# Performance work log

Measured on AMD Instinct MI355X. Metric: run time of the kernel, lower is better.

## Reference

```python
import jax, jax.numpy as jnp
import numpy as np

NG, ND = 50000, 20000
EG, ED = 300000, 150000
FG = FD = 256
H = 256
FC = 2048
B = 65536
EPS = 1e-5


def _lrelu(x):
    return jnp.where(x >= 0, x, 0.01 * x)


def _bn(x, g, b):
    # BatchNorm1d in training mode: biased batch stats over the node dim
    m = x.mean(axis=0)
    v = ((x - m) ** 2).mean(axis=0)
    return (x - m) * jax.lax.rsqrt(v + EPS) * g + b


def _gconv(x, edge_index, Wr, br, Ws, n_nodes):
    # PyG GraphConv: out = lin_rel(sum_{j->i} x_j) + lin_root(x_i)
    src, dst = edge_index[0], edge_index[1]
    agg = jax.ops.segment_sum(x[src], dst, num_segments=n_nodes)  # [N, in]
    return agg @ Wr + br + x @ Ws


def setup_inputs() -> dict:
    key = jax.random.key(0)
    ks = iter(jax.random.split(key, 64))
    d = {}
    d["gene_x"] = jax.random.normal(next(ks), (NG, FG), jnp.float32)
    d["disease_x"] = jax.random.normal(next(ks), (ND, FD), jnp.float32)
    d["gene_edge_index"] = jax.random.randint(next(ks), (2, EG), 0, NG, jnp.int32)
    d["disease_edge_index"] = jax.random.randint(next(ks), (2, ED), 0, ND, jnp.int32)
    d["batch_idx"] = jax.random.randint(next(ks), (B, 2), 0, ND, jnp.int32)

    def lin(fin, fout):
        s = 1.0 / np.sqrt(fin)
        W = jax.random.uniform(next(ks), (fin, fout), jnp.float32, -s, s)
        b = jax.random.uniform(next(ks), (fout,), jnp.float32, -s, s)
        return W, b

    for p, fin in (("g", FG), ("d", FD)):
        for i in range(3):
            f = fin if i == 0 else H
            Wr, br = lin(f, H)
            Ws, _ = lin(f, H)
            d[f"{p}{i}_Wr"], d[f"{p}{i}_br"], d[f"{p}{i}_Ws"] = Wr, br, Ws
            d[f"bn{p}{i}_g"] = jnp.ones((H,), jnp.float32)
            d[f"bn{p}{i}_b"] = jnp.zeros((H,), jnp.float32)
    d["lin1_W"], d["lin1_b"] = lin(2 * H, FC)
    d["lin2_W"], d["lin2_b"] = lin(FC, FC // 2)
    d["lin3_W"], d["lin3_b"] = lin(FC // 2, FC // 4)
    d["lin4_W"], d["lin4_b"] = lin(FC // 4, 2)
    return d


def reference(gene_x, disease_x, gene_edge_index, disease_edge_index, batch_idx,
              g0_Wr, g0_br, g0_Ws, g1_Wr, g1_br, g1_Ws, g2_Wr, g2_br, g2_Ws,
              d0_Wr, d0_br, d0_Ws, d1_Wr, d1_br, d1_Ws, d2_Wr, d2_br, d2_Ws,
              bng0_g, bng0_b, bng1_g, bng1_b, bng2_g, bng2_b,
              bnd0_g, bnd0_b, bnd1_g, bnd1_b, bnd2_g, bnd2_b,
              lin1_W, lin1_b, lin2_W, lin2_b, lin3_W, lin3_b, lin4_W, lin4_b):
    # gene tower
    g0 = _bn(_lrelu(_gconv(gene_x, gene_edge_index, g0_Wr, g0_br, g0_Ws, NG)), bng0_g, bng0_b)
    g1 = _bn(_lrelu(_gconv(g0, gene_edge_index, g1_Wr, g1_br, g1_Ws, NG)), bng1_g, bng1_b)
    g2 = _bn(_lrelu(_gconv(g1, gene_edge_index, g2_Wr, g2_br, g2_Ws, NG)), bng2_g, bng2_b)
    gene_out = 0.7 * g0 + 0.2 * g1 + 0.1 * g2
    # disease tower
    h0 = _bn(_lrelu(_gconv(disease_x, disease_edge_index, d0_Wr, d0_br, d0_Ws, ND)), bnd0_g, bnd0_b)
    h1 = _bn(_lrelu(_gconv(h0, disease_edge_index, d1_Wr, d1_br, d1_Ws, ND)), bnd1_g, bnd1_b)
    h2 = _bn(_lrelu(_gconv(h1, disease_edge_index, d2_Wr, d2_br, d2_Ws, ND)), bnd2_g, bnd2_b)
    dis_out = 0.7 * h0 + 0.2 * h1 + 0.1 * h2
    # pair gather + MLP head (dropout is identity in eval)
    x = jnp.concatenate([gene_out[batch_idx[:, 0]], dis_out[batch_idx[:, 1]]], axis=1)
    x = _lrelu(x @ lin1_W + lin1_b)
    x = _lrelu(x @ lin2_W + lin2_b)
    x = _lrelu(x @ lin3_W + lin3_b)
    return x @ lin4_W + lin4_b
```

## Files before the change

### kernel.cpp

```cpp
#include <hip/hip_runtime.h>
#include <hip/hip_bf16.h>
#include <cstdint>
#include <cstddef>

#define N_G 50000
#define N_D 20000
#define E_G 300000
#define E_D 150000
#define BATCH 65536

typedef _Float16 f16;
typedef _Float16 f16x8 __attribute__((ext_vector_type(8)));
typedef _Float16 f16x4 __attribute__((ext_vector_type(4)));
typedef float f32x4 __attribute__((ext_vector_type(4)));

__device__ __forceinline__ float clampf(float v) {
    return fminf(fmaxf(v, -60000.f), 60000.f);
}

__device__ __forceinline__ void gl_lds16(const void* g, void* l) {
    __builtin_amdgcn_global_load_lds(
        (const __attribute__((address_space(1))) unsigned int*)g,
        (__attribute__((address_space(3))) unsigned int*)l, 16, 0, 0);
}

__global__ __launch_bounds__(256) void gemm_f16(
    const f16* __restrict__ A,
    const int* __restrict__ bidx,
    const f16* __restrict__ geneT, const f16* __restrict__ disT, int rowBase,
    const f16* __restrict__ Bt, const float* __restrict__ bias,
    f16* __restrict__ C, int M, int N, int K, int relu, int CB, int RB,
    const float* __restrict__ W4, float* __restrict__ outF)
{
    alignas(16) __shared__ f16 sA[128 * 64];
    alignas(16) __shared__ f16 sB[128 * 64];
    const int t = threadIdx.x;
    const int w = t >> 6, l = t & 63;
    const int wm = w >> 1, wn = w & 1;
    const int q = l >> 4, lr = l & 15;

    int flat = blockIdx.x;
    int cb, rb;
    if ((RB & 7) == 0) {
        int x = flat & 7, idx = flat >> 3;
        int Sx = RB >> 3;
        cb = idx % CB;
        rb = x * Sx + idx / CB;
    } else {
        cb = flat % CB;
        rb = flat / CB;
    }
    const int mBase = rb * 128, nBase = cb * 128;

    const int subrow = l >> 3;
    const int c = l & 7;
    const char* pA[4];
    const char* pD[4];
    const char* pB[4];
    const bool fused = (bidx != nullptr);
    const bool concat = (!fused && disT != nullptr);
    const bool twoSrc = fused || concat;
#pragma unroll
    for (int j = 0; j < 4; j++) {
        int seg = j * 4 + w;
        int lrow = seg * 8 + subrow;
        int coff = ((c ^ (lrow & 7)) << 4);
        if (fused) {
            int rg = rowBase + mBase + lrow;
            int gi = bidx[2 * rg], di = bidx[2 * rg + 1];
            pA[j] = (const char*)geneT + (size_t)gi * 512 + coff;
            pD[j] = (const char*)disT + (size_t)di * 512 + coff;
        } else if (concat) {
            int arow = mBase + lrow; if (arow > M - 1) arow = M - 1;
            pA[j] = (const char*)geneT + (size_t)arow * 512 + coff;
            pD[j] = (const char*)disT + (size_t)arow * 512 + coff;
        } else {
            int arow = mBase + lrow; if (arow > M - 1) arow = M - 1;
            pA[j] = (const char*)A + (size_t)arow * K * 2 + coff;
            pD[j] = nullptr;
        }
        int brow = nBase + lrow; if (brow > N - 1) brow = N - 1;
        pB[j] = (const char*)Bt + (size_t)brow * K * 2 + coff;
    }

    f32x4 acc[4][4] = {};

    for (int k0 = 0; k0 < K; k0 += 64) {
        __syncthreads();
#pragma unroll
        for (int j = 0; j < 4; j++) {
            int seg = j * 4 + w;
            const char* srcA;
            if (twoSrc)
                srcA = (k0 < 256) ? (pA[j] + (size_t)k0 * 2) : (pD[j] + (size_t)(k0 - 256) * 2);
            else
                srcA = pA[j] + (size_t)k0 * 2;
            gl_lds16(srcA, sA + seg * 512);
            gl_lds16(pB[j] + (size_t)k0 * 2, sB + seg * 512);
        }
        __syncthreads();
        f16x8 a0[4], a1[4], b0[4], b1[4];
#pragma unroll
        for (int i = 0; i < 4; i++) {
            int r = wm * 64 + i * 16 + lr;
            int rs = r * 64;
            int x0 = (q ^ (r & 7)) << 3;
            int x1 = ((4 + q) ^ (r & 7)) << 3;
            a0[i] = *(const f16x8*)(sA + rs + x0);
            a1[i] = *(const f16x8*)(sA + rs + x1);
        }
#pragma unroll
        for (int jj = 0; jj < 4; jj++) {
            int r = wn * 64 + jj * 16 + lr;
            int rs = r * 64;
            int x0 = (q ^ (r & 7)) << 3;
            int x1 = ((4 + q) ^ (r & 7)) << 3;
            b0[jj] = *(const f16x8*)(sB + rs + x0);
            b1[jj] = *(const f16x8*)(sB + rs + x1);
        }
#pragma unroll
        for (int i = 0; i < 4; i++)
#pragma unroll
            for (int jj = 0; jj < 4; jj++) {
                acc[i][jj] = __builtin_amdgcn_mfma_f32_16x16x32_f16(a0[i], b0[jj], acc[i][jj], 0, 0, 0);
                acc[i][jj] = __builtin_amdgcn_mfma_f32_16x16x32_f16(a1[i], b1[jj], acc[i][jj], 0, 0, 0);
            }
    }

    if (W4 != nullptr) {
        float w40[4], w41[4];
#pragma unroll
        for (int j = 0; j < 4; j++) {
            int col = nBase + wn * 64 + j * 16 + lr;
            w40[j] = W4[col * 2];
            w41[j] = W4[col * 2 + 1];
        }
#pragma unroll
        for (int i = 0; i < 4; i++) {
#pragma unroll
            for (int r = 0; r < 4; r++) {
                int row = mBase + wm * 64 + i * 16 + q * 4 + r;
                float s0 = 0.f, s1 = 0.f;
#pragma unroll
                for (int j = 0; j < 4; j++) {
                    int col = nBase + wn * 64 + j * 16 + lr;
                    float v = acc[i][j][r] + bias[col];
                    v = v >= 0.f ? v : 0.01f * v;
                    v = clampf(v);
                    s0 += v * w40[j];
                    s1 += v * w41[j];
                }
#pragma unroll
                for (int off = 1; off < 16; off <<= 1) {
                    s0 += __shfl_xor(s0, off);
                    s1 += __shfl_xor(s1, off);
                }
                if (lr == 0 && row < M) {
                    atomicAdd(&outF[(size_t)(rowBase + row) * 2], s0);
                    atomicAdd(&outF[(size_t)(rowBase + row) * 2 + 1], s1);
                }
            }
        }
        return;
    }

    __syncthreads();
    f16* lt = ((w >> 1) ? sB : sA) + (w & 1) * 4096;

    float bj[4];
#pragma unroll
    for (int j = 0; j < 4; j++)
        bj[j] = bias ? bias[nBase + wn * 64 + j * 16 + lr] : 0.f;

#pragma unroll
    for (int i = 0; i < 4; i++)
#pragma unroll
        for (int j = 0; j < 4; j++) {
            int col = j * 16 + lr;
#pragma unroll
            for (int r = 0; r < 4; r++) {
                int row = i * 16 + q * 4 + r;
                float v = acc[i][j][r] + bj[j];
                if (relu) v = v >= 0.f ? v : 0.01f * v;
                v = clampf(v);
                int cs = col ^ ((((row >> 2) & 3) << 4) ^ ((row & 3) << 3));
                lt[row * 64 + cs] = (f16)v;
            }
        }
    __syncthreads();

    const int rr = l >> 3;
    const int c8 = l & 7;
#pragma unroll
    for (int it = 0; it < 8; it++) {
        int row = it * 8 + rr;
        int cs = (c8 * 8) ^ ((((row >> 2) & 3) << 4) ^ ((row & 3) << 3));
        f16x8 vv = *(const f16x8*)(lt + row * 64 + cs);
        int grow = mBase + wm * 64 + row;
        if (grow < M)
            *(f16x8*)(C + (size_t)grow * N + nBase + wn * 64 + c8 * 8) = vv;
    }
}

__global__ __launch_bounds__(512) void gemm256(
    const f16* __restrict__ A,
    const int* __restrict__ bidx,
    const f16* __restrict__ geneT, const f16* __restrict__ disT, int rowBase,
    const f16* __restrict__ Bt, const float* __restrict__ bias,
    f16* __restrict__ C, int M, int N, int K, int relu, int CB, int RB)
{
    alignas(16) __shared__ f16 sm[81920];
    const int t = threadIdx.x;
    const int w = t >> 6, l = t & 63;
    const int wm = w >> 2, wn = w & 3;
    const int q = l >> 4, lr = l & 15;

    int flat = blockIdx.x;
    int cb, rb;
    if ((RB & 7) == 0) {
        int x = flat & 7, idx = flat >> 3;
        int Sx = RB >> 3;
        cb = idx % CB;
        rb = x * Sx + idx / CB;
    } else {
        cb = flat % CB;
        rb = flat / CB;
    }
    const int mBase = rb * 256, nBase = cb * 256;

    const int subrow = l >> 3;
    const int c = l & 7;
    const bool gat = (bidx != nullptr);
    const char* pA[4];
    const char* pD[4];
    const char* pB[4];
#pragma unroll
    for (int jj = 0; jj < 4; jj++) {
        int arow = jj * 64 + w * 8 + subrow;
        int coff = ((c ^ (arow & 7)) << 4);
        if (gat) {
            int rg = rowBase + mBase + arow;
            int gi = bidx[2 * rg], di = bidx[2 * rg + 1];
            pA[jj] = (const char*)geneT + (size_t)gi * 512 + coff;
            pD[jj] = (const char*)disT + (size_t)di * 512 + coff;
        } else {
            int ga = mBase + arow; if (ga > M - 1) ga = M - 1;
            pA[jj] = (const char*)A + (size_t)ga * K * 2 + coff;
            pD[jj] = nullptr;
        }
        int gb = nBase + arow; if (gb > N - 1) gb = N - 1;
        pB[jj] = (const char*)Bt + (size_t)gb * K * 2 + coff;
    }

    f16* const smA = sm;
    f16* const smB = sm + 3 * 16384;

    auto stageA = [&](int abuf, int k0) {
        f16* bA = smA + abuf * 16384;
#pragma unroll
        for (int jj = 0; jj < 4; jj++) {
            int R0 = jj * 64 + w * 8;
            const char* srcA;
            if (gat)
                srcA = (k0 < 256) ? (pA[jj] + (size_t)k0 * 2) : (pD[jj] + (size_t)(k0 - 256) * 2);
            else
                srcA = pA[jj] + (size_t)k0 * 2;
            gl_lds16(srcA, bA + R0 * 64);
        }
    };
    auto stageB = [&](int bbuf, int k0) {
        f16* bB = smB + bbuf * 16384;
#pragma unroll
        for (int jj = 0; jj < 4; jj++) {
            int R0 = jj * 64 + w * 8;
            gl_lds16(pB[jj] + (size_t)k0 * 2, bB + R0 * 64);
        }
    };

    f32x4 acc[8][4] = {};
    const int nkt = K >> 6;

    stageA(0, 0);
    stageB(0, 0);
    if (nkt > 1) stageA(1, 64);

    for (int kt = 0; kt < nkt; kt++) {
        if (kt + 1 < nkt) stageB((kt + 1) & 1, (kt + 1) << 6);
        if (kt + 2 < nkt) stageA((kt + 2) % 3, (kt + 2) << 6);
        if (kt + 2 < nkt)      asm volatile("s_waitcnt vmcnt(12)" ::: "memory");
        else if (kt + 1 < nkt) asm volatile("s_waitcnt vmcnt(8)" ::: "memory");
        else                   asm volatile("s_waitcnt vmcnt(0)" ::: "memory");
        __builtin_amdgcn_s_barrier();
        __builtin_amdgcn_sched_barrier(0);
        const f16* bA = smA + (kt % 3) * 16384;
        const f16* bB = smB + (kt & 1) * 16384;
#pragma unroll
        for (int ks = 0; ks < 2; ks++) {
            f16x8 bf[4];
#pragma unroll
            for (int nf = 0; nf < 4; nf++) {
                int rB = wn * 64 + nf * 16 + lr;
                bf[nf] = *(const f16x8*)(bB + rB * 64 + ((((ks << 2) + q) ^ (rB & 7)) << 3));
            }
#pragma unroll
            for (int mf = 0; mf < 8; mf++) {
                int rA = wm * 128 + mf * 16 + lr;
                f16x8 af = *(const f16x8*)(bA + rA * 64 + ((((ks << 2) + q) ^ (rA & 7)) << 3));
#pragma unroll
                for (int nf = 0; nf < 4; nf++)
                    acc[mf][nf] = __builtin_amdgcn_mfma_f32_16x16x32_f16(af, bf[nf], acc[mf][nf], 0, 0, 0);
            }
        }
        __builtin_amdgcn_sched_barrier(0);
        __builtin_amdgcn_s_barrier();
    }
    __builtin_amdgcn_sched_barrier(0);

    f16* lt = sm + w * 8192;
    float bj[4];
#pragma unroll
    for (int nf = 0; nf < 4; nf++)
        bj[nf] = bias ? bias[nBase + wn * 64 + nf * 16 + lr] : 0.f;

#pragma unroll
    for (int mf = 0; mf < 8; mf++)
#pragma unroll
        for (int nf = 0; nf < 4; nf++) {
            int col = nf * 16 + lr;
#pragma unroll
            for (int r = 0; r < 4; r++) {
                int row = mf * 16 + q * 4 + r;
                float v = acc[mf][nf][r] + bj[nf];
                if (relu) v = v >= 0.f ? v : 0.01f * v;
                v = clampf(v);
                int cs = col ^ ((((row >> 2) & 3) << 4) ^ ((row & 3) << 3));
                lt[row * 64 + cs] = (f16)v;
            }
        }

    const int rr = l >> 3;
    const int c8 = l & 7;
#pragma unroll
    for (int it = 0; it < 16; it++) {
        int row = it * 8 + rr;
        int cs = (c8 * 8) ^ ((((row >> 2) & 3) << 4) ^ ((row & 3) << 3));
        f16x8 vv = *(const f16x8*)(lt + row * 64 + cs);
        int grow = mBase + wm * 128 + row;
        if (grow < M)
            *(f16x8*)(C + (size_t)grow * N + nBase + wn * 64 + c8 * 8) = vv;
    }
}

__global__ __launch_bounds__(256) void gemm_tower2(
    const f16* __restrict__ Xg, const f16* __restrict__ XAg,
    const f16* __restrict__ Btg, const float* __restrict__ biasg,
    f16* __restrict__ Cg, int Mg, int RBg, float* __restrict__ statsg,
    const f16* __restrict__ Xd, const f16* __restrict__ XAd,
    const f16* __restrict__ Btd, const float* __restrict__ biasd,
    f16* __restrict__ Cd, int Md, int RBd, float* __restrict__ statsd)
{
    alignas(16) __shared__ f16 sA[128 * 64];
    alignas(16) __shared__ f16 sB[128 * 64];
    const int t = threadIdx.x;
    const int w = t >> 6, l = t & 63;
    const int wm = w >> 1, wn = w & 1;
    const int q = l >> 4, lr = l & 15;

    int flat = blockIdx.x;
    const int geneBlocks = 2 * RBg;
    const f16* X;  const f16* XA;  const f16* Bt;  const float* bias;
    f16* C;  int M, RB;  float* stats;
    if (flat < geneBlocks) {
        X = Xg; XA = XAg; Bt = Btg; bias = biasg; C = Cg; M = Mg; RB = RBg; stats = statsg;
    } else {
        flat -= geneBlocks;
        X = Xd; XA = XAd; Bt = Btd; bias = biasd; C = Cd; M = Md; RB = RBd; stats = statsd;
    }

    int cb, rb;
    if ((RB & 7) == 0) {
        int x = flat & 7, idx = flat >> 3;
        int Sx = RB >> 3;
        cb = idx % 2;
        rb = x * Sx + idx / 2;
    } else {
        cb = flat % 2;
        rb = flat / 2;
    }
    const int mBase = rb * 128, nBase = cb * 128;

    const int subrow = l >> 3;
    const int c = l & 7;
    const char* pA[4];
    const char* pD[4];
    const char* pB[4];
#pragma unroll
    for (int j = 0; j < 4; j++) {
        int seg = j * 4 + w;
        int lrow = seg * 8 + subrow;
        int coff = ((c ^ (lrow & 7)) << 4);
        int arow = mBase + lrow; if (arow > M - 1) arow = M - 1;
        pA[j] = (const char*)X + (size_t)arow * 512 + coff;
        pD[j] = (const char*)XA + (size_t)arow * 512 + coff;
        int brow = nBase + lrow; if (brow > 255) brow = 255;
        pB[j] = (const char*)Bt + (size_t)brow * 1024 + coff;
    }

    f32x4 acc[4][4] = {};

    for (int k0 = 0; k0 < 512; k0 += 64) {
        __syncthreads();
#pragma unroll
        for (int j = 0; j < 4; j++) {
            int seg = j * 4 + w;
            const char* srcA = (k0 < 256) ? (pA[j] + (size_t)k0 * 2)
                                          : (pD[j] + (size_t)(k0 - 256) * 2);
            gl_lds16(srcA, sA + seg * 512);
            gl_lds16(pB[j] + (size_t)k0 * 2, sB + seg * 512);
        }
        __syncthreads();
        f16x8 a0[4], a1[4], b0[4], b1[4];
#pragma unroll
        for (int i = 0; i < 4; i++) {
            int r = wm * 64 + i * 16 + lr;
            int rs = r * 64;
            int x0 = (q ^ (r & 7)) << 3;
            int x1 = ((4 + q) ^ (r & 7)) << 3;
            a0[i] = *(const f16x8*)(sA + rs + x0);
            a1[i] = *(const f16x8*)(sA + rs + x1);
        }
#pragma unroll
        for (int jj = 0; jj < 4; jj++) {
            int r = wn * 64 + jj * 16 + lr;
            int rs = r * 64;
            int x0 = (q ^ (r & 7)) << 3;
            int x1 = ((4 + q) ^ (r & 7)) << 3;
            b0[jj] = *(const f16x8*)(sB + rs + x0);
            b1[jj] = *(const f16x8*)(sB + rs + x1);
        }
#pragma unroll
        for (int i = 0; i < 4; i++)
#pragma unroll
            for (int jj = 0; jj < 4; jj++) {
                acc[i][jj] = __builtin_amdgcn_mfma_f32_16x16x32_f16(a0[i], b0[jj], acc[i][jj], 0, 0, 0);
                acc[i][jj] = __builtin_amdgcn_mfma_f32_16x16x32_f16(a1[i], b1[jj], acc[i][jj], 0, 0, 0);
            }
    }

    __syncthreads();
    f16* lt = ((w >> 1) ? sB : sA) + (w & 1) * 4096;

    float bj[4];
#pragma unroll
    for (int j = 0; j < 4; j++)
        bj[j] = bias[nBase + wn * 64 + j * 16 + lr];

    float sj[4] = {0.f, 0.f, 0.f, 0.f}, s2j[4] = {0.f, 0.f, 0.f, 0.f};
#pragma unroll
    for (int i = 0; i < 4; i++)
#pragma unroll
        for (int j = 0; j < 4; j++) {
            int col = j * 16 + lr;
#pragma unroll
            for (int r = 0; r < 4; r++) {
                int row = i * 16 + q * 4 + r;
                float v = acc[i][j][r] + bj[j];
                v = v >= 0.f ? v : 0.01f * v;
                v = clampf(v);
                if ((mBase + wm * 64 + row) < M) { sj[j] += v; s2j[j] += v * v; }
                int cs = col ^ ((((row >> 2) & 3) << 4) ^ ((row & 3) << 3));
                lt[row * 64 + cs] = (f16)v;
            }
        }

#pragma unroll
    for (int j = 0; j < 4; j++) {
        float s = sj[j], s2 = s2j[j];
        s += __shfl_xor(s, 16); s2 += __shfl_xor(s2, 16);
        s += __shfl_xor(s, 32); s2 += __shfl_xor(s2, 32);
        if (q == 0) {
            int col = nBase + wn * 64 + j * 16 + lr;
            atomicAdd(&stats[col], s);
            atomicAdd(&stats[256 + col], s2);
        }
    }
    __syncthreads();

    const int rr = l >> 3;
    const int c8 = l & 7;
#pragma unroll
    for (int it = 0; it < 8; it++) {
        int row = it * 8 + rr;
        int cs = (c8 * 8) ^ ((((row >> 2) & 3) << 4) ^ ((row & 3) << 3));
        f16x8 vv = *(const f16x8*)(lt + row * 64 + cs);
        int grow = mBase + wm * 64 + row;
        if (grow < M)
            *(f16x8*)(C + (size_t)grow * 256 + nBase + wn * 64 + c8 * 8) = vv;
    }
}

__global__ void cvt2(const float* __restrict__ gx, const float* __restrict__ dx,
                     f16* __restrict__ og, f16* __restrict__ od) {
    size_t i = ((size_t)blockIdx.x * 256 + threadIdx.x) * 8;
    const size_t ng = (size_t)N_G * 256;
    const float* in; f16* out;
    if (i < ng) { in = gx + i; out = og + i; }
    else {
        size_t j = i - ng;
        if (j >= (size_t)N_D * 256) return;
        in = dx + j; out = od + j;
    }
    f32x4 a = *(const f32x4*)in;
    f32x4 b = *(const f32x4*)(in + 4);
    f16x8 o;
    o[0] = (f16)clampf(a.x); o[1] = (f16)clampf(a.y);
    o[2] = (f16)clampf(a.z); o[3] = (f16)clampf(a.w);
    o[4] = (f16)clampf(b.x); o[5] = (f16)clampf(b.y);
    o[6] = (f16)clampf(b.z); o[7] = (f16)clampf(b.w);
    *(f16x8*)out = o;
}

__global__ void init_out(const float* __restrict__ b4, float* __restrict__ out, int n) {
    int i = blockIdx.x * 256 + threadIdx.x;
    if (i < n) out[i] = b4[i & 1];
}

__global__ void count_deg2(const int* __restrict__ gei, const int* __restrict__ dei,
                           int* __restrict__ cntg, int* __restrict__ cntd) {
    int e = blockIdx.x * 256 + threadIdx.x;
    if (e < E_G) atomicAdd(&cntg[gei[E_G + e]], 1);
    else if (e < E_G + E_D) atomicAdd(&cntd[dei[E_D + (e - E_G)]], 1);
}

__global__ void scan_deg2(const int* __restrict__ cntg, int* __restrict__ rpg,
                          const int* __restrict__ cntd, int* __restrict__ rpd) {
    __shared__ int part[1024];
    const int t = threadIdx.x;
    const int* deg = blockIdx.x ? cntd : cntg;
    int* rowptr = blockIdx.x ? rpd : rpg;
    const int Nn = blockIdx.x ? N_D : N_G;
    const int C = (Nn + 1023) >> 10;
    const int base = t * C;
    int s = 0;
    for (int i = 0; i < C; i++) { int idx = base + i; if (idx < Nn) s += deg[idx]; }
    part[t] = s;
    __syncthreads();
    for (int off = 1; off < 1024; off <<= 1) {
        int v = (t >= off) ? part[t - off] : 0;
        __syncthreads();
        part[t] += v;
        __syncthreads();
    }
    int pre = (t == 0) ? 0 : part[t - 1];
    for (int i = 0; i < C; i++) {
        int idx = base + i;
        if (idx < Nn) { rowptr[idx] = pre; pre += deg[idx]; }
    }
    if (t == 1023) rowptr[Nn] = part[1023];
}

__global__ void fill_csr2(const int* __restrict__ gei, const int* __restrict__ dei,
                          const int* __restrict__ rpg, const int* __restrict__ rpd,
                          int* __restrict__ curg, int* __restrict__ curd,
                          int* __restrict__ csrg, int* __restrict__ csrd) {
    int e = blockIdx.x * 256 + threadIdx.x;
    if (e < E_G) {
        int d = gei[E_G + e];
        int p = rpg[d] + atomicAdd(&curg[d], 1);
        csrg[p] = gei[e];
    } else if (e < E_G + E_D) {
        int e2 = e - E_G;
        int d = dei[E_D + e2];
        int p = rpd[d] + atomicAdd(&curd[d], 1);
        csrd[p] = dei[e2];
    }
}

__global__ void agg_x2(const int* __restrict__ rpg, const int* __restrict__ csrg,
                       const f16* __restrict__ Xg, f16* __restrict__ XAg,
                       const int* __restrict__ rpd, const int* __restrict__ csrd,
                       const f16* __restrict__ Xd, f16* __restrict__ XAd) {
    int gid = blockIdx.x * 256 + threadIdx.x;
    int node = gid >> 6, l = gid & 63;
    const int* rowptr; const int* csr; const f16* X; f16* XA;
    if (node < N_G) { rowptr = rpg; csr = csrg; X = Xg; XA = XAg; }
    else {
        node -= N_G;
        if (node >= N_D) return;
        rowptr = rpd; csr = csrd; X = Xd; XA = XAd;
    }
    int beg = rowptr[node], end = rowptr[node + 1];
    float s0 = 0.f, s1 = 0.f, s2 = 0.f, s3 = 0.f;
    for (int e = beg; e < end; e++) {
        int src = csr[e];
        f16x4 xv = *(const f16x4*)(X + (size_t)src * 256 + l * 4);
        s0 += (float)xv.x; s1 += (float)xv.y; s2 += (float)xv.z; s3 += (float)xv.w;
    }
    f16x4 o;
    o.x = (f16)clampf(s0); o.y = (f16)clampf(s1);
    o.z = (f16)clampf(s2); o.w = (f16)clampf(s3);
    *(f16x4*)(XA + (size_t)node * 256 + l * 4) = o;
}

__global__ void bn_apply2(f16* __restrict__ yg, f16* __restrict__ yd,
                          const float* __restrict__ stg, const float* __restrict__ std_,
                          const float* __restrict__ gg, const float* __restrict__ bg,
                          const float* __restrict__ gd, const float* __restrict__ bd,
                          float invNg, float invNd, float wv,
                          f16* __restrict__ accg, f16* __restrict__ accd, int initAcc) {
    size_t i = ((size_t)blockIdx.x * 256 + threadIdx.x) * 8;
    const size_t ng = (size_t)N_G * 256;
    f16* y; f16* acc; const float* stats; const float* g; const float* b; float invN;
    if (i < ng) { y = yg + i; acc = accg + i; stats = stg; g = gg; b = bg; invN = invNg; }
    else {
        size_t j = i - ng;
        if (j >= (size_t)N_D * 256) return;
        y = yd + j; acc = accd + j; stats = std_; g = gd; b = bd; invN = invNd;
    }
    int colb = (int)(i & 255);
    f16x8 yv = *(const f16x8*)y;
    f16x8 av = {};
    if (!initAcc) av = *(const f16x8*)acc;
    f16x8 yo, ao;
#pragma unroll
    for (int j = 0; j < 8; j++) {
        int col = colb + j;
        float m = stats[col] * invN;
        float var = stats[256 + col] * invN - m * m;
        if (var < 0.f) var = 0.f;
        float rs = 1.0f / sqrtf(var + 1e-5f);
        float v = ((float)yv[j] - m) * rs * g[col] + b[col];
        v = clampf(v);
        yo[j] = (f16)v;
        float p = initAcc ? 0.f : (float)av[j];
        ao[j] = (f16)clampf(p + wv * v);
    }
    *(f16x8*)y = yo;
    *(f16x8*)acc = ao;
}

__global__ void transpose_tile(const float* __restrict__ W, f16* __restrict__ WT,
                               int K, int N, int dstRowOff, int dstColOff, int LK) {
    __shared__ float tile[32][33];
    int n0 = blockIdx.x * 32, k0 = blockIdx.y * 32;
    int tx = threadIdx.x, ty = threadIdx.y;
    for (int yy = ty; yy < 32; yy += 8) {
        int k = k0 + yy, n = n0 + tx;
        tile[yy][tx] = (k < K && n < N) ? W[(size_t)k * N + n] : 0.f;
    }
    __syncthreads();
    for (int yy = ty; yy < 32; yy += 8) {
        int n = n0 + yy, k = k0 + tx;
        if (n < N && k < K)
            WT[(size_t)(dstRowOff + n) * LK + dstColOff + k] = (f16)clampf(tile[tx][yy]);
    }
}

struct WPtrs { const float* p[12]; };
__global__ void transpose12(WPtrs wp, f16* __restrict__ WT) {
    __shared__ float tile[32][33];
    const int z = blockIdx.z;
    const float* W = wp.p[z];
    const int s = z >> 1;
    const int colOff = (z & 1) * 256;
    f16* dst = WT + (size_t)s * 131072;
    int n0 = blockIdx.x * 32, k0 = blockIdx.y * 32;
    int tx = threadIdx.x, ty = threadIdx.y;
    for (int yy = ty; yy < 32; yy += 8)
        tile[yy][tx] = W[(size_t)(k0 + yy) * 256 + n0 + tx];
    __syncthreads();
    for (int yy = ty; yy < 32; yy += 8)
        dst[(size_t)(n0 + yy) * 512 + colOff + k0 + tx] = (f16)clampf(tile[tx][yy]);
}

extern "C" void kernel_launch(void* const* d_in, const int* in_sizes, int n_in,
                              void* d_out, int out_size, void* d_ws, size_t ws_size,
                              hipStream_t stream) {
    char* ws = (char*)d_ws;
    size_t off = 0;
    auto alloc = [&](size_t bytes) -> void* {
        void* p = ws + off;
        off += (bytes + 255) & ~(size_t)255;
        return p;
    };

    f16* gene_out = (f16*)alloc((size_t)N_G * 256 * 2);
    f16* dis_out  = (f16*)alloc((size_t)N_D * 256 * 2);
    f16* W1T = (f16*)alloc((size_t)2048 * 512 * 2);
    f16* W2T = (f16*)alloc((size_t)1024 * 2048 * 2);
    f16* W3T = (f16*)alloc((size_t)512 * 1024 * 2);
    f16* WcatT = (f16*)alloc((size_t)6 * 256 * 512 * 2);
    int* csr_g = (int*)alloc((size_t)E_G * 4);
    int* csr_d = (int*)alloc((size_t)E_D * 4);
    int* rp_g = (int*)alloc((size_t)(N_G + 1) * 4);
    int* rp_d = (int*)alloc((size_t)(N_D + 1) * 4);
    int* cnt = (int*)alloc((size_t)(N_G + N_D) * 4);
    int* cnt_g = cnt;
    int* cnt_d = cnt + N_G;
    float* statsAll = (float*)alloc(6 * 512 * 4);

    char* scratch = ws + off;
    size_t avail = (ws_size > off) ? (ws_size - off) : 0;

    const size_t NSG = (size_t)N_G * 256;
    const size_t NSD = (size_t)N_D * 256;
    f16* gX = (f16*)scratch;
    f16* gY = gX + NSG;
    f16* gXA = gY + NSG;
    f16* dX = gXA + NSG;
    f16* dY = dX + NSD;
    f16* dXA = dY + NSD;

    int R = BATCH;
    while ((size_t)R * 6144 > avail && R > 256) R >>= 1;
    int chunks = BATCH / R;
    f16* h1 = (f16*)scratch;
    f16* h2 = h1 + (size_t)R * 2048;

    const float* gene_x = (const float*)d_in[0];
    const float* disease_x = (const float*)d_in[1];
    const int* g_ei = (const int*)d_in[2];
    const int* d_ei = (const int*)d_in[3];
    const int* bidx = (const int*)d_in[4];
    float* out = (float*)d_out;

    const float wl[3] = {0.7f, 0.2f, 0.1f};

    hipMemsetAsync(statsAll, 0, 6 * 512 * 4, stream);
    hipMemsetAsync(cnt, 0, (size_t)(N_G + N_D) * 4, stream);
    {
        size_t tot8 = ((NSG + NSD) / 8 + 255) / 256;
        cvt2<<<(int)tot8, 256, 0, stream>>>(gene_x, disease_x, gX, dX);
    }
    count_deg2<<<(E_G + E_D + 255) / 256, 256, 0, stream>>>(g_ei, d_ei, cnt_g, cnt_d);
    scan_deg2<<<2, 1024, 0, stream>>>(cnt_g, rp_g, cnt_d, rp_d);
    hipMemsetAsync(cnt, 0, (size_t)(N_G + N_D) * 4, stream);
    fill_csr2<<<(E_G + E_D + 255) / 256, 256, 0, stream>>>(g_ei, d_ei, rp_g, rp_d,
                                                           cnt_g, cnt_d, csr_g, csr_d);
    {
        WPtrs wp;
        for (int l = 0; l < 3; l++) {
            wp.p[l * 2 + 0] = (const float*)d_in[5 + l * 5 + 2];
            wp.p[l * 2 + 1] = (const float*)d_in[5 + l * 5 + 0];
            wp.p[6 + l * 2 + 0] = (const float*)d_in[20 + l * 5 + 2];
            wp.p[6 + l * 2 + 1] = (const float*)d_in[20 + l * 5 + 0];
        }
        transpose12<<<dim3(8, 8, 12), dim3(32, 8), 0, stream>>>(wp, WcatT);
    }

    const int RBg = ((N_G + 127) / 128 + 7) & ~7;
    const int RBd = ((N_D + 127) / 128 + 7) & ~7;
    f16* gIn = gX; f16* gOut = gY;
    f16* dIn = dX; f16* dOut = dY;
    int aggBlocks = ((N_G + N_D) * 64 + 255) / 256;
    int bnBlocks = (int)(((NSG + NSD) / 8 + 255) / 256);
    for (int l = 0; l < 3; l++) {
        const float* br_g = (const float*)d_in[5 + l * 5 + 1];
        const float* bg_g = (const float*)d_in[5 + l * 5 + 3];
        const float* bb_g = (const float*)d_in[5 + l * 5 + 4];
        const float* br_d = (const float*)d_in[20 + l * 5 + 1];
        const float* bg_d = (const float*)d_in[20 + l * 5 + 3];
        const float* bb_d = (const float*)d_in[20 + l * 5 + 4];
        agg_x2<<<aggBlocks, 256, 0, stream>>>(rp_g, csr_g, gIn, gXA,
                                              rp_d, csr_d, dIn, dXA);
        gemm_tower2<<<2 * RBg + 2 * RBd, 256, 0, stream>>>(
            gIn, gXA, WcatT + (size_t)l * 131072, br_g, gOut, N_G, RBg, statsAll + l * 512,
            dIn, dXA, WcatT + (size_t)(3 + l) * 131072, br_d, dOut, N_D, RBd,
            statsAll + (3 + l) * 512);
        bn_apply2<<<bnBlocks, 256, 0, stream>>>(gOut, dOut,
                                                statsAll + l * 512, statsAll + (3 + l) * 512,
                                                bg_g, bb_g, bg_d, bb_d,
                                                1.0f / N_G, 1.0f / N_D, wl[l],
                                                gene_out, dis_out, l == 0);
        f16* tmp = gIn; gIn = gOut; gOut = tmp;
        tmp = dIn; dIn = dOut; dOut = tmp;
    }

    const float* lin1_W = (const float*)d_in[35];
    const float* lin1_b = (const float*)d_in[36];
    const float* lin2_W = (const float*)d_in[37];
    const float* lin2_b = (const float*)d_in[38];
    const float* lin3_W = (const float*)d_in[39];
    const float* lin3_b = (const float*)d_in[40];
    const float* lin4_W = (const float*)d_in[41];
    const float* lin4_b = (const float*)d_in[42];

    transpose_tile<<<dim3(64, 16), dim3(32, 8), 0, stream>>>(lin1_W, W1T, 512, 2048, 0, 0, 512);
    transpose_tile<<<dim3(32, 64), dim3(32, 8), 0, stream>>>(lin2_W, W2T, 2048, 1024, 0, 0, 2048);
    transpose_tile<<<dim3(16, 32), dim3(32, 8), 0, stream>>>(lin3_W, W3T, 1024, 512, 0, 0, 1024);
    init_out<<<(BATCH * 2 + 255) / 256, 256, 0, stream>>>(lin4_b, out, BATCH * 2);

    for (int c = 0; c < chunks; c++) {
        int rb = c * R;
        int RB = R / 128;
        if ((R & 255) == 0) {
            int RB2 = R / 256;
            gemm256<<<8 * RB2, 512, 0, stream>>>(nullptr, bidx, gene_out, dis_out, rb,
                                                 W1T, lin1_b, h1, R, 2048, 512, 1, 8, RB2);
        } else {
            gemm_f16<<<16 * RB, 256, 0, stream>>>(nullptr, bidx, gene_out, dis_out, rb,
                                                  W1T, lin1_b, h1, R, 2048, 512, 1, 16, RB,
                                                  nullptr, nullptr);
        }
        gemm_f16<<<8 * RB, 256, 0, stream>>>(h1, nullptr, nullptr, nullptr, 0,
                                             W2T, lin2_b, h2, R, 1024, 2048, 1, 8, RB,
                                             nullptr, nullptr);
        gemm_f16<<<4 * RB, 256, 0, stream>>>(h2, nullptr, nullptr, nullptr, rb,
                                             W3T, lin3_b, nullptr, R, 512, 1024, 1, 4, RB,
                                             lin4_W, out);
    }
}
```

Baseline: 1.328 ms.

## Replace 256x256 pipelined lin1 GEMM with 128x512 wide-tile single-buffer kernel

The lin1 GEMM, which gathers gene and disease rows, now uses a 128x512 output tile per 512-thread block, with each wave covering all 128 rows and its own 64 columns. The old version used 256x256 tiles with triple/double-buffered async staging. Shared memory drops from 160KB to 80KB, which should allow more blocks per CU and reduce gathered A-row loads per output column. The cost is that the software pipelining across k-tiles is removed: loads and compute are now serialized by __syncthreads each iteration. The epilogue is also split into two halves so it fits in the smaller LDS.

```diff
diff --git a/kernel.cpp b/kernel.cpp
--- a/kernel.cpp
+++ b/kernel.cpp
@@ -202,18 +202,19 @@
     }
 }
 
-__global__ __launch_bounds__(512) void gemm256(
-    const f16* __restrict__ A,
+__global__ __launch_bounds__(512) void gemm_wide(
     const int* __restrict__ bidx,
     const f16* __restrict__ geneT, const f16* __restrict__ disT, int rowBase,
     const f16* __restrict__ Bt, const float* __restrict__ bias,
-    f16* __restrict__ C, int M, int N, int K, int relu, int CB, int RB)
+    f16* __restrict__ C, int M, int N, int K, int CB, int RB)
 {
-    alignas(16) __shared__ f16 sm[81920];
+    alignas(16) __shared__ f16 sm[40960];
+    f16* const sA = sm;
+    f16* const sB = sm + 8192;
     const int t = threadIdx.x;
     const int w = t >> 6, l = t & 63;
-    const int wm = w >> 2, wn = w & 3;
     const int q = l >> 4, lr = l & 15;
+    const int subrow = l >> 3, c = l & 7;
 
     int flat = blockIdx.x;
     int cb, rb;
@@ -226,128 +227,99 @@
         cb = flat % CB;
         rb = flat / CB;
     }
-    const int mBase = rb * 256, nBase = cb * 256;
-
-    const int subrow = l >> 3;
-    const int c = l & 7;
-    const bool gat = (bidx != nullptr);
-    const char* pA[4];
-    const char* pD[4];
-    const char* pB[4];
-#pragma unroll
-    for (int jj = 0; jj < 4; jj++) {
-        int arow = jj * 64 + w * 8 + subrow;
-        int coff = ((c ^ (arow & 7)) << 4);
-        if (gat) {
-            int rg = rowBase + mBase + arow;
-            int gi = bidx[2 * rg], di = bidx[2 * rg + 1];
-            pA[jj] = (const char*)geneT + (size_t)gi * 512 + coff;
-            pD[jj] = (const char*)disT + (size_t)di * 512 + coff;
-        } else {
-            int ga = mBase + arow; if (ga > M - 1) ga = M - 1;
-            pA[jj] = (const char*)A + (size_t)ga * K * 2 + coff;
-            pD[jj] = nullptr;
-        }
-        int gb = nBase + arow; if (gb > N - 1) gb = N - 1;
-        pB[jj] = (const char*)Bt + (size_t)gb * K * 2 + coff;
-    }
-
-    f16* const smA = sm;
-    f16* const smB = sm + 3 * 16384;
-
-    auto stageA = [&](int abuf, int k0) {
-        f16* bA = smA + abuf * 16384;
-#pragma unroll
-        for (int jj = 0; jj < 4; jj++) {
-            int R0 = jj * 64 + w * 8;
-            const char* srcA;
-            if (gat)
-                srcA = (k0 < 256) ? (pA[jj] + (size_t)k0 * 2) : (pD[jj] + (size_t)(k0 - 256) * 2);
-            else
-                srcA = pA[jj] + (size_t)k0 * 2;
-            gl_lds16(srcA, bA + R0 * 64);
-        }
-    };
-    auto stageB = [&](int bbuf, int k0) {
-        f16* bB = smB + bbuf * 16384;
-#pragma unroll
-        for (int jj = 0; jj < 4; jj++) {
-            int R0 = jj * 64 + w * 8;
-            gl_lds16(pB[jj] + (size_t)k0 * 2, bB + R0 * 64);
-        }
-    };
+    const int mBase = rb * 128, nBase = cb * 512;
+
+    const char* pA[2];
+    const char* pD[2];
+#pragma unroll
+    for (int j = 0; j < 2; j++) {
+        int row = (w * 2 + j) * 8 + subrow;
+        int coff = ((c ^ (row & 7)) << 4);
+        int rg = rowBase + mBase + row;
+        int gi = bidx[2 * rg], di = bidx[2 * rg + 1];
+        pA[j] = (const char*)geneT + (size_t)gi * 512 + coff;
+        pD[j] = (const char*)disT + (size_t)di * 512 + coff;
+    }
+    const char* pB[8];
+#pragma unroll
+    for (int jj = 0; jj < 8; jj++) {
+        int row = (jj * 8 + w) * 8 + subrow;
+        int coff = ((c ^ (row & 7)) << 4);
+        int brow = nBase + row; if (brow > N - 1) brow = N - 1;
+        pB[jj] = (const char*)Bt + (size_t)brow * K * 2 + coff;
+    }
 
     f32x4 acc[8][4] = {};
-    const int nkt = K >> 6;
-
-    stageA(0, 0);
-    stageB(0, 0);
-    if (nkt > 1) stageA(1, 64);
-
-    for (int kt = 0; kt < nkt; kt++) {
-        if (kt + 1 < nkt) stageB((kt + 1) & 1, (kt + 1) << 6);
-        if (kt + 2 < nkt) stageA((kt + 2) % 3, (kt + 2) << 6);
-        if (kt + 2 < nkt)      asm volatile("s_waitcnt vmcnt(12)" ::: "memory");
-        else if (kt + 1 < nkt) asm volatile("s_waitcnt vmcnt(8)" ::: "memory");
-        else                   asm volatile("s_waitcnt vmcnt(0)" ::: "memory");
-        __builtin_amdgcn_s_barrier();
-        __builtin_amdgcn_sched_barrier(0);
-        const f16* bA = smA + (kt % 3) * 16384;
-        const f16* bB = smB + (kt & 1) * 16384;
+
+    for (int k0 = 0; k0 < K; k0 += 64) {
+        __syncthreads();
+#pragma unroll
+        for (int j = 0; j < 2; j++) {
+            const char* srcA = (k0 < 256) ? (pA[j] + (size_t)k0 * 2)
+                                          : (pD[j] + (size_t)(k0 - 256) * 2);
+            gl_lds16(srcA, sA + (w * 2 + j) * 512);
+        }
+#pragma unroll
+        for (int jj = 0; jj < 8; jj++)
+            gl_lds16(pB[jj] + (size_t)k0 * 2, sB + (jj * 8 + w) * 512);
+        __syncthreads();
 #pragma unroll
         for (int ks = 0; ks < 2; ks++) {
             f16x8 bf[4];
 #pragma unroll
             for (int nf = 0; nf < 4; nf++) {
-                int rB = wn * 64 + nf * 16 + lr;
-                bf[nf] = *(const f16x8*)(bB + rB * 64 + ((((ks << 2) + q) ^ (rB & 7)) << 3));
+                int rB = w * 64 + nf * 16 + lr;
+                bf[nf] = *(const f16x8*)(sB + rB * 64 + ((((ks << 2) + q) ^ (rB & 7)) << 3));
             }
 #pragma unroll
             for (int mf = 0; mf < 8; mf++) {
-                int rA = wm * 128 + mf * 16 + lr;
-                f16x8 af = *(const f16x8*)(bA + rA * 64 + ((((ks << 2) + q) ^ (rA & 7)) << 3));
+                int rA = mf * 16 + lr;
+                f16x8 af = *(const f16x8*)(sA + rA * 64 + ((((ks << 2) + q) ^ (rA & 7)) << 3));
 #pragma unroll
                 for (int nf = 0; nf < 4; nf++)
                     acc[mf][nf] = __builtin_amdgcn_mfma_f32_16x16x32_f16(af, bf[nf], acc[mf][nf], 0, 0, 0);
             }
         }
-        __builtin_amdgcn_sched_barrier(0);
-        __builtin_amdgcn_s_barrier();
-    }
-    __builtin_amdgcn_sched_barrier(0);
-
-    f16* lt = sm + w * 8192;
+    }
+
+    f16* lt = sm + w * 4096;
     float bj[4];
 #pragma unroll
     for (int nf = 0; nf < 4; nf++)
-        bj[nf] = bias ? bias[nBase + wn * 64 + nf * 16 + lr] : 0.f;
-
-#pragma unroll
-    for (int mf = 0; mf < 8; mf++)
-#pragma unroll
-        for (int nf = 0; nf < 4; nf++) {
-            int col = nf * 16 + lr;
-#pragma unroll
-            for (int r = 0; r < 4; r++) {
-                int row = mf * 16 + q * 4 + r;
-                float v = acc[mf][nf][r] + bj[nf];
-                if (relu) v = v >= 0.f ? v : 0.01f * v;
-                v = clampf(v);
-                int cs = col ^ ((((row >> 2) & 3) << 4) ^ ((row & 3) << 3));
-                lt[row * 64 + cs] = (f16)v;
-            }
-        }
+        bj[nf] = bias[nBase + w * 64 + nf * 16 + lr];
 
     const int rr = l >> 3;
     const int c8 = l & 7;
 #pragma unroll
-    for (int it = 0; it < 16; it++) {
-        int row = it * 8 + rr;
-        int cs = (c8 * 8) ^ ((((row >> 2) & 3) << 4) ^ ((row & 3) << 3));
-        f16x8 vv = *(const f16x8*)(lt + row * 64 + cs);
-        int grow = mBase + wm * 128 + row;
-        if (grow < M)
-            *(f16x8*)(C + (size_t)grow * N + nBase + wn * 64 + c8 * 8) = vv;
+    for (int half = 0; half < 2; half++) {
+        __syncthreads();
+#pragma unroll
+        for (int mh = 0; mh < 4; mh++) {
+            int mf = half * 4 + mh;
+#pragma unroll
+            for (int nf = 0; nf < 4; nf++) {
+                int col = nf * 16 + lr;
+#pragma unroll
+                for (int r = 0; r < 4; r++) {
+                    int row = mh * 16 + q * 4 + r;
+                    float v = acc[mf][nf][r] + bj[nf];
+                    v = v >= 0.f ? v : 0.01f * v;
+                    v = clampf(v);
+                    int cs = col ^ ((((row >> 2) & 3) << 4) ^ ((row & 3) << 3));
+                    lt[row * 64 + cs] = (f16)v;
+                }
+            }
+        }
+        __syncthreads();
+#pragma unroll
+        for (int it = 0; it < 8; it++) {
+            int row = it * 8 + rr;
+            int cs = (c8 * 8) ^ ((((row >> 2) & 3) << 4) ^ ((row & 3) << 3));
+            f16x8 vv = *(const f16x8*)(lt + row * 64 + cs);
+            int grow = mBase + half * 64 + row;
+            if (grow < M)
+                *(f16x8*)(C + (size_t)grow * N + nBase + w * 64 + c8 * 8) = vv;
+        }
     }
 }
 
@@ -793,10 +765,9 @@
     for (int c = 0; c < chunks; c++) {
         int rb = c * R;
         int RB = R / 128;
-        if ((R & 255) == 0) {
-            int RB2 = R / 256;
-            gemm256<<<8 * RB2, 512, 0, stream>>>(nullptr, bidx, gene_out, dis_out, rb,
-                                                 W1T, lin1_b, h1, R, 2048, 512, 1, 8, RB2);
+        if ((R & 127) == 0) {
+            gemm_wide<<<4 * RB, 512, 0, stream>>>(bidx, gene_out, dis_out, rb,
+                                                  W1T, lin1_b, h1, R, 2048, 512, 4, RB);
         } else {
             gemm_f16<<<16 * RB, 256, 0, stream>>>(nullptr, bidx, gene_out, dis_out, rb,
                                                   W1T, lin1_b, h1, R, 2048, 512, 1, 16, RB,
```

Result: slower. 1.378 ms, median of 2 (+3.7%).
